# Kernel tuning notes

Measured on AMD Instinct MI355X. Metric: run time of the kernel, lower is better.

## Reference

```python
import jax, jax.numpy as jnp
import numpy as np

DIM = 768
HEADS = 12
DH = DIM // HEADS  # 64


def setup_inputs() -> dict:
    key = jax.random.key(0)
    k1, k2, k3, k4, k5 = jax.random.split(key, 5)
    b, p = 16, 1024
    x = jax.random.normal(k1, (b, p, DIM), dtype=jnp.float32)
    # torch nn.Linear params: W [out, in], b [out]
    s_qkv = 1.0 / np.sqrt(DIM)
    Wqkv = jax.random.uniform(k2, (3 * DIM, DIM), jnp.float32, -s_qkv, s_qkv)
    bqkv = jax.random.uniform(k3, (3 * DIM,), jnp.float32, -s_qkv, s_qkv)
    Wo = jax.random.uniform(k4, (DIM, DIM), jnp.float32, -s_qkv, s_qkv)
    bo = jax.random.uniform(k5, (DIM,), jnp.float32, -s_qkv, s_qkv)
    return {"x": x, "Wqkv": Wqkv, "bqkv": bqkv, "Wo": Wo, "bo": bo}


def reference(x, Wqkv, bqkv, Wo, bo):
    b, p, _ = x.shape
    qkv = x @ Wqkv.T + bqkv                      # [b, p, 3*dim]
    q, k, v = jnp.split(qkv, 3, axis=-1)
    def to_heads(t):
        return t.reshape(b, p, HEADS, DH).transpose(0, 2, 1, 3)  # [b, h, p, d]
    q, k, v = to_heads(q), to_heads(k), to_heads(v)
    A = jnp.einsum('bhqd,bhkd->bhqk', q, k) / jnp.sqrt(jnp.float32(DH))
    # NOTE: softmax over the QUERY axis (dim=2), not the key axis
    P = jax.nn.softmax(A, axis=2)                # [b, h, q, k]
    MSA = jnp.einsum('bhqk,bhkd->bhqd', P, v)    # [b, h, p, d]
    MSA = MSA.transpose(0, 2, 1, 3).reshape(b, p, DIM)
    return MSA @ Wo.T + bo
```

## Files before the change

kernel.cpp:

```cpp
#include <hip/hip_runtime.h>
#include <hip/hip_bf16.h>
#include <math.h>

#define DIMC 768
#define HEADS 12
#define DHD 64
#define NB 16
#define NP 1024
#define NQKV (3*DIMC)

typedef __attribute__((ext_vector_type(8))) short bf16x8;
typedef __attribute__((ext_vector_type(4))) float f32x4;

__device__ __forceinline__ short f2bf(float f){
  unsigned u = __builtin_bit_cast(unsigned, f);
  u = (u + 0x7fffu + ((u >> 16) & 1u)) >> 16;
  return (short)u;
}
__device__ __forceinline__ float bf2f(short s){
  return __builtin_bit_cast(float, ((unsigned)(unsigned short)s) << 16);
}
__device__ __forceinline__ bf16x8 cvt8(float4 a, float4 b){
  bf16x8 v;
  v[0]=f2bf(a.x); v[1]=f2bf(a.y); v[2]=f2bf(a.z); v[3]=f2bf(a.w);
  v[4]=f2bf(b.x); v[5]=f2bf(b.y); v[6]=f2bf(b.z); v[7]=f2bf(b.w);
  return v;
}
__device__ __forceinline__ void glds16(const void* gsrc, void* ldst){
  __builtin_amdgcn_global_load_lds(
      (const __attribute__((address_space(1))) unsigned int*)gsrc,
      (__attribute__((address_space(3))) unsigned int*)ldst, 16, 0, 0);
}
__device__ __forceinline__ int xcd_swz(int p, int nwg){
  return (p & 7) * (nwg >> 3) + (p >> 3);
}

__global__ __launch_bounds__(256) void cvt_bf16(const float* __restrict__ in, short* __restrict__ out, int n8)
{
  int i = blockIdx.x*256 + threadIdx.x;
  if (i < n8) {
    float4 f0 = ((const float4*)in)[i*2];
    float4 f1 = ((const float4*)in)[i*2+1];
    ((bf16x8*)out)[i] = cvt8(f0, f1);
  }
}

template<int OUTBF16, int QSCALE>
__global__ __launch_bounds__(256) void gemm_bt(
    const short* __restrict__ A, const short* __restrict__ B,
    const float* __restrict__ bias, void* __restrict__ Cp,
    int N, int K, int NX)
{
  __shared__ __align__(16) short As[128*32];
  __shared__ __align__(16) short Bs[128*32];
  const int l = xcd_swz(blockIdx.x, gridDim.x);
  const int bn = (l % NX) * 128, bm = (l / NX) * 128;
  const int t = threadIdx.x;
  const int lane = t & 63, w = t >> 6;
  const int wr = w >> 1, wc = w & 1;
  const int lr = lane & 15, lg = lane >> 4;
  const int srow = lane >> 2;
  const int acol = (lane & 3) * 8;

  f32x4 acc[4][4] = {};

  for (int k0 = 0; k0 < K; k0 += 32) {
    glds16(A + (size_t)(bm + w*32 +  0 + srow)*K + k0 + acol, &As[(w*32 +  0)*32]);
    glds16(A + (size_t)(bm + w*32 + 16 + srow)*K + k0 + acol, &As[(w*32 + 16)*32]);
    glds16(B + (size_t)(bn + w*32 +  0 + srow)*K + k0 + acol, &Bs[(w*32 +  0)*32]);
    glds16(B + (size_t)(bn + w*32 + 16 + srow)*K + k0 + acol, &Bs[(w*32 + 16)*32]);
    __syncthreads();
    bf16x8 a[4], b[4];
    #pragma unroll
    for (int i=0;i<4;i++) a[i] = *(const bf16x8*)&As[(wr*64 + i*16 + lr)*32 + lg*8];
    #pragma unroll
    for (int i=0;i<4;i++) b[i] = *(const bf16x8*)&Bs[(wc*64 + i*16 + lr)*32 + lg*8];
    #pragma unroll
    for (int mf=0;mf<4;mf++)
      #pragma unroll
      for (int nf=0;nf<4;nf++)
        acc[mf][nf] = __builtin_amdgcn_mfma_f32_16x16x32_bf16(a[mf], b[nf], acc[mf][nf], 0,0,0);
    __syncthreads();
  }
  #pragma unroll
  for (int nf=0;nf<4;nf++){
    const int n = bn + wc*64 + nf*16 + lr;
    const float bb = bias[n];
    const float sc = (QSCALE && n < DIMC) ? 0.18033688011112042f : 1.0f;
    #pragma unroll
    for (int mf=0;mf<4;mf++)
      #pragma unroll
      for (int i=0;i<4;i++){
        const int m = bm + wr*64 + mf*16 + lg*4 + i;
        const float v = (acc[mf][nf][i] + bb) * sc;
        if (OUTBF16) ((short*)Cp)[(size_t)m*N + n] = f2bf(v);
        else         ((float*)Cp)[(size_t)m*N + n] = v;
      }
  }
}

__global__ __launch_bounds__(256) void vtrans(const short* __restrict__ qkv,
                                              const float* __restrict__ invs,
                                              short* __restrict__ vT)
{
  __shared__ __align__(16) short Ts[64][72];
  __shared__ float invl[64];
  const int pt = blockIdx.x, h = blockIdx.y, b = blockIdx.z;
  const int t = threadIdx.x;
  const size_t bh = (size_t)(b*HEADS + h);
  if (t < 64) invl[t] = invs[bh*NP + pt*64 + t];
  {
    const int r = t >> 2, q = t & 3;
    const short* src = qkv + (size_t)(b*NP + pt*64 + r)*NQKV + 2*DIMC + h*DHD + q*16;
    *(bf16x8*)&Ts[r][q*16]   = *(const bf16x8*)src;
    *(bf16x8*)&Ts[r][q*16+8] = *(const bf16x8*)(src+8);
  }
  __syncthreads();
  {
    const int d = t >> 2, q = t & 3;
    __align__(16) short tmp[16];
    #pragma unroll
    for (int j=0;j<16;j++) tmp[j] = f2bf(bf2f(Ts[q*16 + j][d]) * invl[q*16 + j]);
    short* dst = vT + (bh*DHD + d)*NP + pt*64 + q*16;
    *(bf16x8*)dst     = *(bf16x8*)&tmp[0];
    *(bf16x8*)(dst+8) = *(bf16x8*)&tmp[8];
  }
}

__global__ __launch_bounds__(256) void col_stats(const short* __restrict__ qkv, float* __restrict__ invs)
{
  __shared__ __align__(16) short Ks[128][72];
  __shared__ __align__(16) short Qs[64][72];
  __shared__ float red[4][128];
  const int l = xcd_swz(blockIdx.x, gridDim.x);
  const int kc = l & 7, h = (l >> 3) % HEADS, b = l / (8*HEADS);
  const int t = threadIdx.x;
  const int lane = t & 63, w = t >> 6;
  const int lr = lane & 15, lg = lane >> 4, lk = lg*8;
  const size_t rowbase = (size_t)(b*NP)*NQKV + h*DHD;
  {
    const int r = t >> 1, half = t & 1;
    const short* src = qkv + rowbase + (size_t)(kc*128 + r)*NQKV + DIMC + half*32;
    #pragma unroll
    for (int c=0;c<4;c++)
      *(bf16x8*)&Ks[r][half*32 + c*8] = *(const bf16x8*)(src + c*8);
  }
  float rsum[8] = {};
  for (int qt=0; qt<16; qt++){
    __syncthreads();
    {
      const int r = t >> 2, q = t & 3;
      const short* src = qkv + rowbase + (size_t)(qt*64 + r)*NQKV + q*16;
      *(bf16x8*)&Qs[r][q*16]   = *(const bf16x8*)src;
      *(bf16x8*)&Qs[r][q*16+8] = *(const bf16x8*)(src+8);
    }
    __syncthreads();
    bf16x8 qa0 = *(const bf16x8*)&Qs[w*16 + lr][lk];
    bf16x8 qa1 = *(const bf16x8*)&Qs[w*16 + lr][32 + lk];
    #pragma unroll
    for (int kf=0; kf<8; kf++){
      f32x4 acc = {};
      bf16x8 kb0 = *(const bf16x8*)&Ks[kf*16 + lr][lk];
      bf16x8 kb1 = *(const bf16x8*)&Ks[kf*16 + lr][32 + lk];
      acc = __builtin_amdgcn_mfma_f32_16x16x32_bf16(qa0, kb0, acc, 0,0,0);
      acc = __builtin_amdgcn_mfma_f32_16x16x32_bf16(qa1, kb1, acc, 0,0,0);
      #pragma unroll
      for (int i=0;i<4;i++) rsum[kf] += exp2f(acc[i]);
    }
  }
  #pragma unroll
  for (int kf=0;kf<8;kf++){
    float v = rsum[kf];
    v += __shfl_xor(v, 16);
    v += __shfl_xor(v, 32);
    if (lane < 16) red[w][kf*16 + lr] = v;
  }
  __syncthreads();
  if (t < 128) {
    float s = red[0][t] + red[1][t] + red[2][t] + red[3][t];
    invs[(size_t)(b*HEADS + h)*NP + kc*128 + t] = 1.0f / s;
  }
}

__global__ __launch_bounds__(256) void attn_pv(const short* __restrict__ qkv, const short* __restrict__ vT,
                                               short* __restrict__ msa)
{
  __shared__ __align__(16) short Ks[64*64];
  __shared__ __align__(16) short Vs[64*64];
  __shared__ __align__(16) short Ps[4][16][72];
  const int l = xcd_swz(blockIdx.x, gridDim.x);
  const int qt2 = l & 7, h = (l >> 3) % HEADS, b = l / (8*HEADS);
  const int t = threadIdx.x;
  const int lane = t & 63, w = t >> 6;
  const int lr = lane & 15, lg = lane >> 4;
  const size_t qkvbase = (size_t)(b*NP)*NQKV + h*DHD;
  const size_t bh = (size_t)(b*HEADS + h);
  bf16x8 qa[2][2];
  {
    const short* Qbase = qkv + qkvbase + (size_t)(qt2*128 + w*32 + lr)*NQKV + lg*8;
    #pragma unroll
    for (int g=0; g<2; g++)
      #pragma unroll
      for (int hh=0; hh<2; hh++)
        qa[g][hh] = *(const bf16x8*)(Qbase + (size_t)g*16*NQKV + hh*32);
  }
  const int srw = lane >> 3;
  const int scol = 8 * ((lane & 7) ^ srw);
  const int sx = (lr & 7) << 3;
  const short* Kg = qkv + qkvbase + DIMC;
  const short* Vg = vT + bh*DHD*NP;
  f32x4 o[2][4] = {};
  for (int kt=0; kt<16; kt++){
    #pragma unroll
    for (int j=0; j<2; j++){
      const int r0 = w*16 + j*8;
      glds16(Kg + (size_t)(kt*64 + r0 + srw)*NQKV + scol, &Ks[r0*64]);
      glds16(Vg + (size_t)(r0 + srw)*NP + kt*64 + scol,   &Vs[r0*64]);
    }
    __syncthreads();
    bf16x8 kb[4][2], vb[4][2];
    #pragma unroll
    for (int kf=0; kf<4; kf++)
      #pragma unroll
      for (int hh=0; hh<2; hh++)
        kb[kf][hh] = *(const bf16x8*)&Ks[(kf*16 + lr)*64 + ((hh*32 + lg*8) ^ sx)];
    #pragma unroll
    for (int df=0; df<4; df++)
      #pragma unroll
      for (int kk=0; kk<2; kk++)
        vb[df][kk] = *(const bf16x8*)&Vs[(df*16 + lr)*64 + ((kk*32 + lg*8) ^ sx)];
    #pragma unroll
    for (int g=0; g<2; g++){
      #pragma unroll
      for (int kf=0; kf<4; kf++){
        f32x4 s = {};
        s = __builtin_amdgcn_mfma_f32_16x16x32_bf16(kb[kf][0], qa[g][0], s, 0,0,0);
        s = __builtin_amdgcn_mfma_f32_16x16x32_bf16(kb[kf][1], qa[g][1], s, 0,0,0);
        float e0 = exp2f(s[0]), e1 = exp2f(s[1]), e2 = exp2f(s[2]), e3 = exp2f(s[3]);
        unsigned u0, u1;
        asm("v_cvt_pk_bf16_f32 %0, %1, %2" : "=v"(u0) : "v"(e0), "v"(e1));
        asm("v_cvt_pk_bf16_f32 %0, %1, %2" : "=v"(u1) : "v"(e2), "v"(e3));
        uint2 uu; uu.x = u0; uu.y = u1;
        *(uint2*)&Ps[w][lr][kf*16 + lg*4] = uu;
      }
      bf16x8 pa0 = *(const bf16x8*)&Ps[w][lr][lg*8];
      bf16x8 pa1 = *(const bf16x8*)&Ps[w][lr][32 + lg*8];
      #pragma unroll
      for (int df=0; df<4; df++){
        o[g][df] = __builtin_amdgcn_mfma_f32_16x16x32_bf16(pa0, vb[df][0], o[g][df], 0,0,0);
        o[g][df] = __builtin_amdgcn_mfma_f32_16x16x32_bf16(pa1, vb[df][1], o[g][df], 0,0,0);
      }
    }
    __syncthreads();
  }
  #pragma unroll
  for (int g=0; g<2; g++)
    #pragma unroll
    for (int df=0; df<4; df++){
      const int d = h*DHD + df*16 + lr;
      #pragma unroll
      for (int i=0;i<4;i++){
        const int p = qt2*128 + w*32 + g*16 + lg*4 + i;
        msa[((size_t)(b*NP) + p)*DIMC + d] = f2bf(o[g][df][i]);
      }
    }
}

extern "C" void kernel_launch(void* const* d_in, const int* in_sizes, int n_in,
                              void* d_out, int out_size, void* d_ws, size_t ws_size,
                              hipStream_t stream)
{
  const float* x    = (const float*)d_in[0];
  const float* Wqkv = (const float*)d_in[1];
  const float* bqkv = (const float*)d_in[2];
  const float* Wo   = (const float*)d_in[3];
  const float* bo   = (const float*)d_in[4];
  char* ws = (char*)d_ws;
  short* qkv   = (short*)ws;
  short* vT    = (short*)(ws + 75497472);
  short* Wqkvb = vT;
  short* msa   = (short*)(ws + 100663296);
  short* xb    = msa;
  float* invs  = (float*)(ws + 125829120);
  short* Wob   = qkv;

  cvt_bf16<<<6144, 256, 0, stream>>>(x, xb, (16384*768)/8);
  cvt_bf16<<<864, 256, 0, stream>>>(Wqkv, Wqkvb, (2304*768)/8);
  gemm_bt<1,1><<<2304, 256, 0, stream>>>(xb, Wqkvb, bqkv, qkv, NQKV, DIMC, 18);
  col_stats<<<1536, 256, 0, stream>>>(qkv, invs);
  vtrans<<<dim3(16, HEADS, NB), 256, 0, stream>>>(qkv, invs, vT);
  attn_pv<<<1536, 256, 0, stream>>>(qkv, vT, msa);
  cvt_bf16<<<288, 256, 0, stream>>>(Wo, Wob, (768*768)/8);
  gemm_bt<0,0><<<768, 256, 0, stream>>>(msa, Wob, bo, d_out, DIMC, DIMC, 6);
}
```

Before: 393.9 us.

## Double-buffer K/V tiles in attn_pv and use native exp2

The attn_pv loop now keeps two LDS buffers for K and V and issues the global-to-LDS loads for the next tile before computing on the current one. Explicit vmcnt waits plus raw barriers replace __syncthreads, so loads overlap with MFMA and exp work. K/V fragments are read from LDS just before use rather than all at once, which lowers register pressure. It also switches exp2f to the hardware exp2 builtin and raises wave priority around the MFMA sections. In exchange, LDS use doubles and the manual waitcnt handling is fragile. The native exp2 may also differ slightly in precision for denormal inputs.

```diff
diff --git a/kernel.cpp b/kernel.cpp
--- a/kernel.cpp
+++ b/kernel.cpp
@@ -165,7 +165,7 @@
       acc = __builtin_amdgcn_mfma_f32_16x16x32_bf16(qa0, kb0, acc, 0,0,0);
       acc = __builtin_amdgcn_mfma_f32_16x16x32_bf16(qa1, kb1, acc, 0,0,0);
       #pragma unroll
-      for (int i=0;i<4;i++) rsum[kf] += exp2f(acc[i]);
+      for (int i=0;i<4;i++) rsum[kf] += __builtin_amdgcn_exp2f(acc[i]);
     }
   }
   #pragma unroll
@@ -185,8 +185,8 @@
 __global__ __launch_bounds__(256) void attn_pv(const short* __restrict__ qkv, const short* __restrict__ vT,
                                                short* __restrict__ msa)
 {
-  __shared__ __align__(16) short Ks[64*64];
-  __shared__ __align__(16) short Vs[64*64];
+  __shared__ __align__(16) short Ks[2][64*64];
+  __shared__ __align__(16) short Vs[2][64*64];
   __shared__ __align__(16) short Ps[4][16][72];
   const int l = xcd_swz(blockIdx.x, gridDim.x);
   const int qt2 = l & 7, h = (l >> 3) % HEADS, b = l / (8*HEADS);
@@ -207,36 +207,47 @@
   const int srw = lane >> 3;
   const int scol = 8 * ((lane & 7) ^ srw);
   const int sx = (lr & 7) << 3;
-  const short* Kg = qkv + qkvbase + DIMC;
-  const short* Vg = vT + bh*DHD*NP;
+  const short* kp = qkv + qkvbase + DIMC + (size_t)(w*16 + srw)*NQKV + scol;
+  const short* vp = vT + bh*DHD*NP + (size_t)(w*16 + srw)*NP + scol;
+
+  #define STAGE(buf, kt) do { \
+    _Pragma("unroll") \
+    for (int j=0; j<2; j++){ \
+      glds16(kp + (size_t)((kt)*64 + j*8)*NQKV, &Ks[buf][(w*16 + j*8)*64]); \
+      glds16(vp + (size_t)(j*8)*NP + (kt)*64,   &Vs[buf][(w*16 + j*8)*64]); \
+    } } while(0)
+
   f32x4 o[2][4] = {};
+  STAGE(0, 0);
+  int cur = 0;
   for (int kt=0; kt<16; kt++){
-    #pragma unroll
-    for (int j=0; j<2; j++){
-      const int r0 = w*16 + j*8;
-      glds16(Kg + (size_t)(kt*64 + r0 + srw)*NQKV + scol, &Ks[r0*64]);
-      glds16(Vg + (size_t)(r0 + srw)*NP + kt*64 + scol,   &Vs[r0*64]);
-    }
-    __syncthreads();
-    bf16x8 kb[4][2], vb[4][2];
-    #pragma unroll
-    for (int kf=0; kf<4; kf++)
-      #pragma unroll
-      for (int hh=0; hh<2; hh++)
-        kb[kf][hh] = *(const bf16x8*)&Ks[(kf*16 + lr)*64 + ((hh*32 + lg*8) ^ sx)];
-    #pragma unroll
-    for (int df=0; df<4; df++)
-      #pragma unroll
-      for (int kk=0; kk<2; kk++)
-        vb[df][kk] = *(const bf16x8*)&Vs[(df*16 + lr)*64 + ((kk*32 + lg*8) ^ sx)];
+    if (kt < 15) {
+      STAGE(cur^1, kt+1);
+      asm volatile("s_waitcnt vmcnt(4)" ::: "memory");
+    } else {
+      asm volatile("s_waitcnt vmcnt(0)" ::: "memory");
+    }
+    __builtin_amdgcn_s_barrier();
     #pragma unroll
     for (int g=0; g<2; g++){
+      bf16x8 kb0, kb1;
+      f32x4 s[4];
+      __builtin_amdgcn_s_setprio(1);
       #pragma unroll
       for (int kf=0; kf<4; kf++){
-        f32x4 s = {};
-        s = __builtin_amdgcn_mfma_f32_16x16x32_bf16(kb[kf][0], qa[g][0], s, 0,0,0);
-        s = __builtin_amdgcn_mfma_f32_16x16x32_bf16(kb[kf][1], qa[g][1], s, 0,0,0);
-        float e0 = exp2f(s[0]), e1 = exp2f(s[1]), e2 = exp2f(s[2]), e3 = exp2f(s[3]);
+        kb0 = *(const bf16x8*)&Ks[cur][(kf*16 + lr)*64 + ((     lg*8) ^ sx)];
+        kb1 = *(const bf16x8*)&Ks[cur][(kf*16 + lr)*64 + ((32 + lg*8) ^ sx)];
+        f32x4 z = {};
+        z = __builtin_amdgcn_mfma_f32_16x16x32_bf16(kb0, qa[g][0], z, 0,0,0);
+        s[kf] = __builtin_amdgcn_mfma_f32_16x16x32_bf16(kb1, qa[g][1], z, 0,0,0);
+      }
+      __builtin_amdgcn_s_setprio(0);
+      #pragma unroll
+      for (int kf=0; kf<4; kf++){
+        float e0 = __builtin_amdgcn_exp2f(s[kf][0]);
+        float e1 = __builtin_amdgcn_exp2f(s[kf][1]);
+        float e2 = __builtin_amdgcn_exp2f(s[kf][2]);
+        float e3 = __builtin_amdgcn_exp2f(s[kf][3]);
         unsigned u0, u1;
         asm("v_cvt_pk_bf16_f32 %0, %1, %2" : "=v"(u0) : "v"(e0), "v"(e1));
         asm("v_cvt_pk_bf16_f32 %0, %1, %2" : "=v"(u1) : "v"(e2), "v"(e3));
@@ -245,14 +256,20 @@
       }
       bf16x8 pa0 = *(const bf16x8*)&Ps[w][lr][lg*8];
       bf16x8 pa1 = *(const bf16x8*)&Ps[w][lr][32 + lg*8];
+      __builtin_amdgcn_s_setprio(1);
       #pragma unroll
       for (int df=0; df<4; df++){
-        o[g][df] = __builtin_amdgcn_mfma_f32_16x16x32_bf16(pa0, vb[df][0], o[g][df], 0,0,0);
-        o[g][df] = __builtin_amdgcn_mfma_f32_16x16x32_bf16(pa1, vb[df][1], o[g][df], 0,0,0);
-      }
-    }
-    __syncthreads();
-  }
+        bf16x8 vb0 = *(const bf16x8*)&Vs[cur][(df*16 + lr)*64 + ((     lg*8) ^ sx)];
+        bf16x8 vb1 = *(const bf16x8*)&Vs[cur][(df*16 + lr)*64 + ((32 + lg*8) ^ sx)];
+        o[g][df] = __builtin_amdgcn_mfma_f32_16x16x32_bf16(pa0, vb0, o[g][df], 0,0,0);
+        o[g][df] = __builtin_amdgcn_mfma_f32_16x16x32_bf16(pa1, vb1, o[g][df], 0,0,0);
+      }
+      __builtin_amdgcn_s_setprio(0);
+    }
+    __builtin_amdgcn_s_barrier();
+    cur ^= 1;
+  }
+  #undef STAGE
   #pragma unroll
   for (int g=0; g<2; g++)
     #pragma unroll
```

Measured after the change: 347.5 us. 1.13x faster.
